# Performance work log

Hardware: AMD Instinct MI355X
Metric: run time of the kernel (lower is better)

Reference implementation:

```python
import jax, jax.numpy as jnp
import numpy as np
import math

C = 128
LAM = 0.25
MARGIN = 0.3
TAU = math.log(C)
B = 8192


def lambertw(z, iters=10):
    """Principal-branch Lambert W via Halley iterations (valid for z >= -1/e)."""
    e = jnp.exp(1.0)
    # series init near the branch point z = -1/e, log init for z >= 0
    p = jnp.sqrt(jnp.maximum(2.0 * (e * z + 1.0), 0.0))
    w_near = -1.0 + p - p * p / 3.0 + (11.0 / 72.0) * p ** 3
    w = jnp.where(z < 0.0, w_near, jnp.log1p(jnp.maximum(z, 0.0)))
    for _ in range(iters):
        ew = jnp.exp(w)
        f = w * ew - z
        wp1 = w + 1.0
        w = w - f / (ew * wp1 - (w + 2.0) * f / (2.0 * wp1))
    return w


def triplet_loss(x, targets):
    # pairwise euclidean distances [B, B]
    sq = jnp.sum(x * x, axis=1)
    dist = sq[:, None] + sq[None, :] - 2.0 * (x @ x.T)
    dist = jnp.sqrt(jnp.maximum(dist, 1e-12))
    pos = targets[:, None] == targets[None, :]
    # hardest positive / hardest negative per anchor
    dist_ap = jnp.max(jnp.where(pos, dist, -jnp.inf), axis=1)
    dist_an = jnp.min(jnp.where(pos, jnp.inf, dist), axis=1)
    # MarginRankingLoss(margin)(dist_an, dist_ap, y=1), mean reduction
    return jnp.mean(jnp.maximum(dist_ap - dist_an + MARGIN, 0.0))


def cross_entropy(logits, targets):
    logp = jax.nn.log_softmax(logits, axis=-1)
    return -jnp.mean(jnp.take_along_axis(logp, targets[:, None], axis=1)[:, 0])


def setup_inputs() -> dict:
    key = jax.random.key(0)
    k1, k2 = jax.random.split(key)
    logits = jax.random.normal(k1, (B, C), dtype=jnp.float32)
    targets = jax.random.randint(k2, (B,), 0, C, dtype=jnp.int64)
    return {"logits": logits, "targets": targets}


def reference(logits, targets):
    # l_i is detached in the original (and sigma goes through numpy -> no grad)
    l_i = jax.lax.stop_gradient(triplet_loss(logits, targets))
    y = 0.5 * jnp.maximum(-2.0 / jnp.exp(1.0), (l_i - TAU) / LAM)
    sigma = jax.lax.stop_gradient(jnp.exp(-lambertw(y)))
    ce = cross_entropy(logits, targets)
    loss = (ce - TAU) * sigma + LAM * jnp.log(sigma) ** 2
    return jnp.sum(loss) / B
```

## Files before the change

kernel.cpp:

```cpp
#include <hip/hip_runtime.h>
#include <math.h>

#define NB 8192
#define NC 128
#define NJS 8
#define JPT 8

typedef float v4f __attribute__((ext_vector_type(4)));
typedef int   v8i __attribute__((ext_vector_type(8)));

__global__ __launch_bounds__(256) void k_prep(const float* __restrict__ x,
                                              const int* __restrict__ tgt,
                                              unsigned* __restrict__ xq,
                                              float* __restrict__ sq,
                                              float* __restrict__ ce,
                                              float* __restrict__ sums,
                                              unsigned* __restrict__ cnt) {
    int row = blockIdx.x * 8 + (threadIdx.x >> 5);
    int l = threadIdx.x & 31;
    float4 v = ((const float4*)(x + row * NC))[l];
    unsigned p = __builtin_amdgcn_cvt_pk_fp8_f32(v.x, v.y, 0, false);
    p = __builtin_amdgcn_cvt_pk_fp8_f32(v.z, v.w, p, true);
    xq[row * 32 + l] = p;

    float ss = fmaf(v.x, v.x, fmaf(v.y, v.y, fmaf(v.z, v.z, v.w * v.w)));
    float mx = fmaxf(fmaxf(v.x, v.y), fmaxf(v.z, v.w));
#pragma unroll
    for (int off = 16; off; off >>= 1) {
        ss += __shfl_xor(ss, off);
        mx = fmaxf(mx, __shfl_xor(mx, off));
    }
    float es = expf(v.x - mx) + expf(v.y - mx) + expf(v.z - mx) + expf(v.w - mx);
#pragma unroll
    for (int off = 16; off; off >>= 1) es += __shfl_xor(es, off);
    if (l == 0) {
        sq[row] = ss;
        ce[row] = mx + logf(es) - x[row * NC + tgt[row]];
    }
    if (blockIdx.x == 0 && threadIdx.x < 4) {
        if (threadIdx.x < 2) sums[threadIdx.x] = 0.0f;
        if (threadIdx.x == 2) *cnt = 0u;
    }
}

__global__ __launch_bounds__(256, 4) void k_trip(const unsigned char* __restrict__ xq,
                                                 const int* __restrict__ tgt,
                                                 const float* __restrict__ sq,
                                                 float* __restrict__ pmax,
                                                 float* __restrict__ pmin) {
    __shared__ unsigned char Bs[2][128 * 128];
    __shared__ float sqs[1024];
    __shared__ int   tjs[1024];

    const int tid = threadIdx.x;
    const int lane = tid & 63;
    const int w = tid >> 6;
    const int rh = w >> 1;
    const int ch = w & 1;
    const int i0 = blockIdx.x * 64;
    const int jbase = blockIdx.y * 1024;
    const int m = lane & 15;
    const int quad = lane >> 4;

    __builtin_amdgcn_global_load_lds(
        (const __attribute__((address_space(1))) unsigned*)((const unsigned*)(sq + jbase) + (w * 64 + lane) * 4),
        (__attribute__((address_space(3))) unsigned*)(sqs + w * 256),
        16, 0, 0);
    __builtin_amdgcn_global_load_lds(
        (const __attribute__((address_space(1))) unsigned*)((const unsigned*)(tgt + jbase) + (w * 64 + lane) * 4),
        (__attribute__((address_space(3))) unsigned*)(tjs + w * 256),
        16, 0, 0);

#pragma unroll
    for (int c = 0; c < 4; ++c) {
        int L = w * 256 + c * 64 + lane;
        int col = L >> 3, cc = L & 7;
        const unsigned char* src = xq + (size_t)(jbase + col) * 128 + ((cc ^ (col & 7)) << 4);
        __builtin_amdgcn_global_load_lds(
            (const __attribute__((address_space(1))) unsigned*)src,
            (__attribute__((address_space(3))) unsigned*)(&Bs[0][0] + (w * 256 + c * 64) * 16),
            16, 0, 0);
    }

    v8i a[2];
#pragma unroll
    for (int tm = 0; tm < 2; ++tm) {
        int row = i0 + rh * 32 + tm * 16 + m;
        a[tm] = *(const v8i*)(xq + (size_t)row * 128 + quad * 32);
    }

    int ti[2][4];
#pragma unroll
    for (int tm = 0; tm < 2; ++tm)
#pragma unroll
        for (int r = 0; r < 4; ++r)
            ti[tm][r] = tgt[i0 + rh * 32 + tm * 16 + quad * 4 + r];

    float mp[2][4], mn[2][4];
#pragma unroll
    for (int tm = 0; tm < 2; ++tm)
#pragma unroll
        for (int r = 0; r < 4; ++r) { mp[tm][r] = -3.0e38f; mn[tm][r] = 3.0e38f; }

#pragma unroll 2
    for (int jt = 0; jt < JPT; ++jt) {
        __syncthreads();

        if (jt + 1 < JPT) {
            int jn = jbase + (jt + 1) * 128;
            unsigned char* Bnxt = &Bs[(jt + 1) & 1][0];
#pragma unroll
            for (int c = 0; c < 4; ++c) {
                int L = w * 256 + c * 64 + lane;
                int col = L >> 3, cc = L & 7;
                const unsigned char* src = xq + (size_t)(jn + col) * 128 + ((cc ^ (col & 7)) << 4);
                __builtin_amdgcn_global_load_lds(
                    (const __attribute__((address_space(1))) unsigned*)src,
                    (__attribute__((address_space(3))) unsigned*)(Bnxt + (w * 256 + c * 64) * 16),
                    16, 0, 0);
            }
        }

        const unsigned char* Bcur = &Bs[jt & 1][0];

        float sqj[4]; int tj[4];
#pragma unroll
        for (int tn = 0; tn < 4; ++tn) {
            int cloc = jt * 128 + ch * 64 + tn * 16 + m;
            sqj[tn] = sqs[cloc];
            tj[tn] = tjs[cloc];
        }

        v8i b[4];
#pragma unroll
        for (int tn = 0; tn < 4; ++tn) {
            int col = ch * 64 + tn * 16 + m;
            int base = col * 128;
            int c0 = (((quad * 2) ^ (col & 7)) << 4);
            int c1 = (((quad * 2 + 1) ^ (col & 7)) << 4);
            *(int4*)&b[tn] = *(const int4*)(Bcur + base + c0);
            *((int4*)&b[tn] + 1) = *(const int4*)(Bcur + base + c1);
        }

        v4f acc[2][4];
        v4f z = {0.0f, 0.0f, 0.0f, 0.0f};
#pragma unroll
        for (int tm = 0; tm < 2; ++tm)
#pragma unroll
            for (int tn = 0; tn < 4; ++tn)
                acc[tm][tn] = __builtin_amdgcn_mfma_scale_f32_16x16x128_f8f6f4(
                    a[tm], b[tn], z, 0, 0, 0, 0x7f7f7f7f, 0, 0x7f7f7f7f);

#pragma unroll
        for (int tn = 0; tn < 4; ++tn) {
#pragma unroll
            for (int tm = 0; tm < 2; ++tm)
#pragma unroll
                for (int r = 0; r < 4; ++r) {
                    float v = fmaf(-2.0f, acc[tm][tn][r], sqj[tn]);
                    bool pos = (tj[tn] == ti[tm][r]);
                    mp[tm][r] = fmaxf(mp[tm][r], pos ? v : -3.0e38f);
                    mn[tm][r] = fminf(mn[tm][r], pos ? 3.0e38f : v);
                }
        }
    }

#pragma unroll
    for (int off = 1; off < 16; off <<= 1) {
#pragma unroll
        for (int tm = 0; tm < 2; ++tm)
#pragma unroll
            for (int r = 0; r < 4; ++r) {
                mp[tm][r] = fmaxf(mp[tm][r], __shfl_xor(mp[tm][r], off));
                mn[tm][r] = fminf(mn[tm][r], __shfl_xor(mn[tm][r], off));
            }
    }
    if (m == 0) {
        int slice = blockIdx.y * 2 + ch;
        float* pm = pmax + (size_t)slice * NB + i0 + rh * 32;
        float* pn = pmin + (size_t)slice * NB + i0 + rh * 32;
#pragma unroll
        for (int tm = 0; tm < 2; ++tm)
#pragma unroll
            for (int r = 0; r < 4; ++r) {
                int rr = tm * 16 + quad * 4 + r;
                pm[rr] = mp[tm][r];
                pn[rr] = mn[tm][r];
            }
    }
}

__global__ __launch_bounds__(256) void k_tail(const float* __restrict__ sq,
                                              const float* __restrict__ ce,
                                              const float* __restrict__ pmax,
                                              const float* __restrict__ pmin,
                                              float* __restrict__ sums,
                                              unsigned* __restrict__ cnt,
                                              float* __restrict__ out) {
    __shared__ float sh[4], sc[4];
    __shared__ unsigned lastFlag;
    const int tid = threadIdx.x;
    int i = blockIdx.x * 256 + tid;

    float vmax = -3.0e38f, vmin = 3.0e38f;
#pragma unroll
    for (int s = 0; s < 16; ++s) {
        vmax = fmaxf(vmax, pmax[s * NB + i]);
        vmin = fminf(vmin, pmin[s * NB + i]);
    }
    float sqi = sq[i];
    float ap = sqrtf(fmaxf(fmaxf(sqi + vmax, 0.0f), 1e-12f));
    float an = sqrtf(fmaxf(fmaxf(sqi + vmin, 0.0f), 1e-12f));
    float hs = fmaxf(ap - an + 0.3f, 0.0f);
    float cs = ce[i];
#pragma unroll
    for (int off = 32; off; off >>= 1) {
        hs += __shfl_xor(hs, off);
        cs += __shfl_xor(cs, off);
    }
    int wv = tid >> 6;
    if ((tid & 63) == 0) { sh[wv] = hs; sc[wv] = cs; }
    __syncthreads();
    if (tid == 0) {
        float H = sh[0] + sh[1] + sh[2] + sh[3];
        float Cs = sc[0] + sc[1] + sc[2] + sc[3];
        atomicAdd(sums + 0, H);
        atomicAdd(sums + 1, Cs);
        __threadfence();
        unsigned prev = atomicAdd(cnt, 1u);
        lastFlag = (prev == (unsigned)(gridDim.x - 1));
    }
    __syncthreads();
    if (!lastFlag || tid != 0) return;

    double H = (double)atomicAdd(sums + 0, 0.0f);
    double Cs = (double)atomicAdd(sums + 1, 0.0f);
    const double E = 2.71828182845904523536;
    const double TAU = log(128.0);
    const double LAMd = 0.25;
    double l = H / (double)NB;
    double cev = Cs / (double)NB;
    double y = 0.5 * fmax(-2.0 / E, (l - TAU) / LAMd);
    double p = sqrt(fmax(2.0 * (E * y + 1.0), 0.0));
    double wn = -1.0 + p - p * p / 3.0 + (11.0 / 72.0) * p * p * p;
    double wlw = (y < 0.0) ? wn : log1p(fmax(y, 0.0));
#pragma unroll
    for (int it = 0; it < 10; ++it) {
        double ew = exp(wlw);
        double f = wlw * ew - y;
        double wp1 = wlw + 1.0;
        wlw = wlw - f / (ew * wp1 - (wlw + 2.0) * f / (2.0 * wp1));
    }
    double sigma = exp(-wlw);
    double lg = log(sigma);
    double loss = (cev - TAU) * sigma + LAMd * lg * lg;
    out[0] = (float)(loss / (double)NB);
}

extern "C" void kernel_launch(void* const* d_in, const int* in_sizes, int n_in,
                              void* d_out, int out_size, void* d_ws, size_t ws_size,
                              hipStream_t stream) {
    const float* x = (const float*)d_in[0];
    const int* tgt = (const int*)d_in[1];
    float* out = (float*)d_out;

    unsigned char* xq = (unsigned char*)d_ws;
    float* sq = (float*)(xq + (size_t)NB * 128);
    float* ce = sq + NB;
    float* sums = ce + NB;
    unsigned* cnt = (unsigned*)(sums + 2);
    float* pmax = (float*)(cnt + 62);
    float* pmin = pmax + (size_t)16 * NB;

    k_prep<<<NB / 8, 256, 0, stream>>>(x, tgt, (unsigned*)xq, sq, ce, sums, cnt);
    dim3 grid(NB / 64, NJS);
    k_trip<<<grid, 256, 0, stream>>>(xq, tgt, sq, pmax, pmin);
    k_tail<<<NB / 256, 256, 0, stream>>>(sq, ce, pmax, pmin, sums, cnt, out);
}
```

Before: 83.90 us.

## Exploit distance-matrix symmetry to compute only the upper-triangle tiles

The triplet kernel now skips blocks below the diagonal and, for each computed tile, also reduces column-wise to produce the hardest positive and negative for the transposed anchors. These column partials go to a separate buffer that the tail kernel merges with the row partials. This roughly halves the MFMA and LDS work. In exchange it adds column reductions, cross-lane shuffles, a much larger partial buffer (256 slices) with more global writes and tail reads, and uneven per-block load.

Result: slower. 151.9 us (+81.0%).

```diff
diff --git a/kernel.cpp b/kernel.cpp
--- a/kernel.cpp
+++ b/kernel.cpp
@@ -3,8 +3,8 @@
 
 #define NB 8192
 #define NC 128
-#define NJS 8
-#define JPT 8
+#define NSL 16
+#define JPT 4
 
 typedef float v4f __attribute__((ext_vector_type(4)));
 typedef int   v8i __attribute__((ext_vector_type(8)));
@@ -46,30 +46,35 @@
 __global__ __launch_bounds__(256, 4) void k_trip(const unsigned char* __restrict__ xq,
                                                  const int* __restrict__ tgt,
                                                  const float* __restrict__ sq,
-                                                 float* __restrict__ pmax,
-                                                 float* __restrict__ pmin) {
+                                                 float* __restrict__ rmax,
+                                                 float* __restrict__ rmin,
+                                                 float* __restrict__ cmax,
+                                                 float* __restrict__ cmin) {
+    const int ib = blockIdx.x;
+    const int s = blockIdx.y;
+    if (ib < 8 * s) return;
+    const int jtmax = min(3, (ib - 8 * s) >> 1);
+
     __shared__ unsigned char Bs[2][128 * 128];
-    __shared__ float sqs[1024];
-    __shared__ int   tjs[1024];
+    __shared__ float sqs[512];
+    __shared__ int   tjs[512];
 
     const int tid = threadIdx.x;
     const int lane = tid & 63;
     const int w = tid >> 6;
     const int rh = w >> 1;
     const int ch = w & 1;
-    const int i0 = blockIdx.x * 64;
-    const int jbase = blockIdx.y * 1024;
+    const int i0 = ib * 64;
+    const int jbase = s * 512;
     const int m = lane & 15;
     const int quad = lane >> 4;
 
-    __builtin_amdgcn_global_load_lds(
-        (const __attribute__((address_space(1))) unsigned*)((const unsigned*)(sq + jbase) + (w * 64 + lane) * 4),
-        (__attribute__((address_space(3))) unsigned*)(sqs + w * 256),
-        16, 0, 0);
-    __builtin_amdgcn_global_load_lds(
-        (const __attribute__((address_space(1))) unsigned*)((const unsigned*)(tgt + jbase) + (w * 64 + lane) * 4),
-        (__attribute__((address_space(3))) unsigned*)(tjs + w * 256),
-        16, 0, 0);
+    if (tid < 128) {
+        float4 s4 = *(const float4*)(sq + jbase + tid * 4);
+        int4 t4 = *(const int4*)(tgt + jbase + tid * 4);
+        *(float4*)&sqs[tid * 4] = s4;
+        *(int4*)&tjs[tid * 4] = t4;
+    }
 
 #pragma unroll
     for (int c = 0; c < 4; ++c) {
@@ -90,11 +95,15 @@
     }
 
     int ti[2][4];
+    float sqr[2][4];
 #pragma unroll
     for (int tm = 0; tm < 2; ++tm)
 #pragma unroll
-        for (int r = 0; r < 4; ++r)
-            ti[tm][r] = tgt[i0 + rh * 32 + tm * 16 + quad * 4 + r];
+        for (int r = 0; r < 4; ++r) {
+            int row = i0 + rh * 32 + tm * 16 + quad * 4 + r;
+            ti[tm][r] = tgt[row];
+            sqr[tm][r] = sq[row];
+        }
 
     float mp[2][4], mn[2][4];
 #pragma unroll
@@ -102,11 +111,10 @@
 #pragma unroll
         for (int r = 0; r < 4; ++r) { mp[tm][r] = -3.0e38f; mn[tm][r] = 3.0e38f; }
 
-#pragma unroll 2
-    for (int jt = 0; jt < JPT; ++jt) {
+    for (int jt = 0; jt <= jtmax; ++jt) {
         __syncthreads();
 
-        if (jt + 1 < JPT) {
+        if (jt < jtmax) {
             int jn = jbase + (jt + 1) * 128;
             unsigned char* Bnxt = &Bs[(jt + 1) & 1][0];
 #pragma unroll
@@ -122,46 +130,64 @@
         }
 
         const unsigned char* Bcur = &Bs[jt & 1][0];
-
-        float sqj[4]; int tj[4];
+        const v4f z = {0.0f, 0.0f, 0.0f, 0.0f};
+
+        float cmx[4], cmn[4];
+#pragma unroll
+        for (int tn = 0; tn < 4; ++tn) { cmx[tn] = -3.0e38f; cmn[tn] = 3.0e38f; }
+
 #pragma unroll
         for (int tn = 0; tn < 4; ++tn) {
-            int cloc = jt * 128 + ch * 64 + tn * 16 + m;
-            sqj[tn] = sqs[cloc];
-            tj[tn] = tjs[cloc];
+            int cloc = ch * 64 + tn * 16 + m;
+            float sqj = sqs[jt * 128 + cloc];
+            int tj = tjs[jt * 128 + cloc];
+
+            v8i b;
+            int base = cloc * 128;
+            *(int4*)&b = *(const int4*)(Bcur + base + ((((quad * 2) ^ (cloc & 7))) << 4));
+            *((int4*)&b + 1) = *(const int4*)(Bcur + base + ((((quad * 2 + 1) ^ (cloc & 7))) << 4));
+
+            v4f acc0 = __builtin_amdgcn_mfma_scale_f32_16x16x128_f8f6f4(
+                a[0], b, z, 0, 0, 0, 0x7f7f7f7f, 0, 0x7f7f7f7f);
+            v4f acc1 = __builtin_amdgcn_mfma_scale_f32_16x16x128_f8f6f4(
+                a[1], b, z, 0, 0, 0, 0x7f7f7f7f, 0, 0x7f7f7f7f);
+
+#pragma unroll
+            for (int r = 0; r < 4; ++r) {
+                {
+                    float d2 = fmaf(-2.0f, acc0[r], sqj);
+                    bool pos = (tj == ti[0][r]);
+                    mp[0][r] = fmaxf(mp[0][r], pos ? d2 : -3.0e38f);
+                    mn[0][r] = fminf(mn[0][r], pos ? 3.0e38f : d2);
+                    float vc = fmaf(-2.0f, acc0[r], sqr[0][r]);
+                    cmx[tn] = fmaxf(cmx[tn], pos ? vc : -3.0e38f);
+                    cmn[tn] = fminf(cmn[tn], pos ? 3.0e38f : vc);
+                }
+                {
+                    float d2 = fmaf(-2.0f, acc1[r], sqj);
+                    bool pos = (tj == ti[1][r]);
+                    mp[1][r] = fmaxf(mp[1][r], pos ? d2 : -3.0e38f);
+                    mn[1][r] = fminf(mn[1][r], pos ? 3.0e38f : d2);
+                    float vc = fmaf(-2.0f, acc1[r], sqr[1][r]);
+                    cmx[tn] = fmaxf(cmx[tn], pos ? vc : -3.0e38f);
+                    cmn[tn] = fminf(cmn[tn], pos ? 3.0e38f : vc);
+                }
+            }
         }
 
-        v8i b[4];
 #pragma unroll
         for (int tn = 0; tn < 4; ++tn) {
-            int col = ch * 64 + tn * 16 + m;
-            int base = col * 128;
-            int c0 = (((quad * 2) ^ (col & 7)) << 4);
-            int c1 = (((quad * 2 + 1) ^ (col & 7)) << 4);
-            *(int4*)&b[tn] = *(const int4*)(Bcur + base + c0);
-            *((int4*)&b[tn] + 1) = *(const int4*)(Bcur + base + c1);
-        }
-
-        v4f acc[2][4];
-        v4f z = {0.0f, 0.0f, 0.0f, 0.0f};
-#pragma unroll
-        for (int tm = 0; tm < 2; ++tm)
-#pragma unroll
-            for (int tn = 0; tn < 4; ++tn)
-                acc[tm][tn] = __builtin_amdgcn_mfma_scale_f32_16x16x128_f8f6f4(
-                    a[tm], b[tn], z, 0, 0, 0, 0x7f7f7f7f, 0, 0x7f7f7f7f);
-
-#pragma unroll
-        for (int tn = 0; tn < 4; ++tn) {
-#pragma unroll
-            for (int tm = 0; tm < 2; ++tm)
-#pragma unroll
-                for (int r = 0; r < 4; ++r) {
-                    float v = fmaf(-2.0f, acc[tm][tn][r], sqj[tn]);
-                    bool pos = (tj[tn] == ti[tm][r]);
-                    mp[tm][r] = fmaxf(mp[tm][r], pos ? v : -3.0e38f);
-                    mn[tm][r] = fminf(mn[tm][r], pos ? 3.0e38f : v);
-                }
+            float x1 = cmx[tn], n1 = cmn[tn];
+            x1 = fmaxf(x1, __shfl_xor(x1, 16));
+            x1 = fmaxf(x1, __shfl_xor(x1, 32));
+            n1 = fminf(n1, __shfl_xor(n1, 16));
+            n1 = fminf(n1, __shfl_xor(n1, 32));
+            if (quad == 0) {
+                int jcol = jbase + jt * 128 + ch * 64 + tn * 16 + m;
+                int slice_c = (((ib - 8 * s - 2 * jt)) << 1) + rh;
+                cmax[(size_t)slice_c * NB + jcol] = x1;
+                cmin[(size_t)slice_c * NB + jcol] = n1;
+            }
         }
     }
 
@@ -176,9 +202,9 @@
             }
     }
     if (m == 0) {
-        int slice = blockIdx.y * 2 + ch;
-        float* pm = pmax + (size_t)slice * NB + i0 + rh * 32;
-        float* pn = pmin + (size_t)slice * NB + i0 + rh * 32;
+        int slice = s * 2 + ch;
+        float* pm = rmax + (size_t)slice * NB + i0 + rh * 32;
+        float* pn = rmin + (size_t)slice * NB + i0 + rh * 32;
 #pragma unroll
         for (int tm = 0; tm < 2; ++tm)
 #pragma unroll
@@ -192,8 +218,10 @@
 
 __global__ __launch_bounds__(256) void k_tail(const float* __restrict__ sq,
                                               const float* __restrict__ ce,
-                                              const float* __restrict__ pmax,
-                                              const float* __restrict__ pmin,
+                                              const float* __restrict__ rmax,
+                                              const float* __restrict__ rmin,
+                                              const float* __restrict__ cmax,
+                                              const float* __restrict__ cmin,
                                               float* __restrict__ sums,
                                               unsigned* __restrict__ cnt,
                                               float* __restrict__ out) {
@@ -203,10 +231,15 @@
     int i = blockIdx.x * 256 + tid;
 
     float vmax = -3.0e38f, vmin = 3.0e38f;
-#pragma unroll
-    for (int s = 0; s < 16; ++s) {
-        vmax = fmaxf(vmax, pmax[s * NB + i]);
-        vmin = fminf(vmin, pmin[s * NB + i]);
+    int nrow = 2 * (i >> 9) + 2;
+    for (int sl = 0; sl < nrow; ++sl) {
+        vmax = fmaxf(vmax, rmax[(size_t)sl * NB + i]);
+        vmin = fminf(vmin, rmin[(size_t)sl * NB + i]);
+    }
+    int ncol = (128 - 2 * (i >> 7)) << 1;
+    for (int sl = 0; sl < ncol; ++sl) {
+        vmax = fmaxf(vmax, cmax[(size_t)sl * NB + i]);
+        vmin = fminf(vmin, cmin[(size_t)sl * NB + i]);
     }
     float sqi = sq[i];
     float ap = sqrtf(fmaxf(fmaxf(sqi + vmax, 0.0f), 1e-12f));
@@ -269,11 +302,13 @@
     float* ce = sq + NB;
     float* sums = ce + NB;
     unsigned* cnt = (unsigned*)(sums + 2);
-    float* pmax = (float*)(cnt + 62);
-    float* pmin = pmax + (size_t)16 * NB;
+    float* rmax = (float*)(cnt + 62);
+    float* rmin = rmax + (size_t)32 * NB;
+    float* cmax = rmin + (size_t)32 * NB;
+    float* cmin = cmax + (size_t)256 * NB;
 
     k_prep<<<NB / 8, 256, 0, stream>>>(x, tgt, (unsigned*)xq, sq, ce, sums, cnt);
-    dim3 grid(NB / 64, NJS);
-    k_trip<<<grid, 256, 0, stream>>>(xq, tgt, sq, pmax, pmin);
-    k_tail<<<NB / 256, 256, 0, stream>>>(sq, ce, pmax, pmin, sums, cnt, out);
+    dim3 grid(NB / 64, NSL);
+    k_trip<<<grid, 256, 0, stream>>>(xq, tgt, sq, rmax, rmin, cmax, cmin);
+    k_tail<<<NB / 256, 256, 0, stream>>>(sq, ce, rmax, rmin, cmax, cmin, sums, cnt, out);
 }
```

## Load B tiles directly from global into registers, dropping LDS staging

Applied to the files above, without the earlier changes.

The triplet-distance kernel no longer stages B columns, squared norms and targets through double-buffered shared memory with async global-to-LDS copies and barriers. Each lane now reads its 32-byte fp8 B fragment, sq and target straight from global memory (mostly L2-resident) inside a fully unrolled loop. This removes the barriers and LDS traffic and lowers LDS use, which may raise occupancy. In exchange it adds redundant global loads across waves and exposes load latency without explicit prefetching.

After: 100.5 us. 19.8% more time.

```diff
diff --git a/kernel.cpp b/kernel.cpp
--- a/kernel.cpp
+++ b/kernel.cpp
@@ -48,10 +48,6 @@
                                                  const float* __restrict__ sq,
                                                  float* __restrict__ pmax,
                                                  float* __restrict__ pmin) {
-    __shared__ unsigned char Bs[2][128 * 128];
-    __shared__ float sqs[1024];
-    __shared__ int   tjs[1024];
-
     const int tid = threadIdx.x;
     const int lane = tid & 63;
     const int w = tid >> 6;
@@ -62,26 +58,6 @@
     const int m = lane & 15;
     const int quad = lane >> 4;
 
-    __builtin_amdgcn_global_load_lds(
-        (const __attribute__((address_space(1))) unsigned*)((const unsigned*)(sq + jbase) + (w * 64 + lane) * 4),
-        (__attribute__((address_space(3))) unsigned*)(sqs + w * 256),
-        16, 0, 0);
-    __builtin_amdgcn_global_load_lds(
-        (const __attribute__((address_space(1))) unsigned*)((const unsigned*)(tgt + jbase) + (w * 64 + lane) * 4),
-        (__attribute__((address_space(3))) unsigned*)(tjs + w * 256),
-        16, 0, 0);
-
-#pragma unroll
-    for (int c = 0; c < 4; ++c) {
-        int L = w * 256 + c * 64 + lane;
-        int col = L >> 3, cc = L & 7;
-        const unsigned char* src = xq + (size_t)(jbase + col) * 128 + ((cc ^ (col & 7)) << 4);
-        __builtin_amdgcn_global_load_lds(
-            (const __attribute__((address_space(1))) unsigned*)src,
-            (__attribute__((address_space(3))) unsigned*)(&Bs[0][0] + (w * 256 + c * 64) * 16),
-            16, 0, 0);
-    }
-
     v8i a[2];
 #pragma unroll
     for (int tm = 0; tm < 2; ++tm) {
@@ -102,66 +78,39 @@
 #pragma unroll
         for (int r = 0; r < 4; ++r) { mp[tm][r] = -3.0e38f; mn[tm][r] = 3.0e38f; }
 
-#pragma unroll 2
+    const v4f z = {0.0f, 0.0f, 0.0f, 0.0f};
+
+#pragma unroll
     for (int jt = 0; jt < JPT; ++jt) {
-        __syncthreads();
-
-        if (jt + 1 < JPT) {
-            int jn = jbase + (jt + 1) * 128;
-            unsigned char* Bnxt = &Bs[(jt + 1) & 1][0];
-#pragma unroll
-            for (int c = 0; c < 4; ++c) {
-                int L = w * 256 + c * 64 + lane;
-                int col = L >> 3, cc = L & 7;
-                const unsigned char* src = xq + (size_t)(jn + col) * 128 + ((cc ^ (col & 7)) << 4);
-                __builtin_amdgcn_global_load_lds(
-                    (const __attribute__((address_space(1))) unsigned*)src,
-                    (__attribute__((address_space(3))) unsigned*)(Bnxt + (w * 256 + c * 64) * 16),
-                    16, 0, 0);
+        int j0 = jbase + jt * 128;
+#pragma unroll
+        for (int tn = 0; tn < 4; ++tn) {
+            int col = j0 + ch * 64 + tn * 16 + m;
+
+            v8i b = *(const v8i*)(xq + (size_t)col * 128 + quad * 32);
+            float sqj = sq[col];
+            int tj = tgt[col];
+
+            v4f acc0 = __builtin_amdgcn_mfma_scale_f32_16x16x128_f8f6f4(
+                a[0], b, z, 0, 0, 0, 0x7f7f7f7f, 0, 0x7f7f7f7f);
+            v4f acc1 = __builtin_amdgcn_mfma_scale_f32_16x16x128_f8f6f4(
+                a[1], b, z, 0, 0, 0, 0x7f7f7f7f, 0, 0x7f7f7f7f);
+
+#pragma unroll
+            for (int r = 0; r < 4; ++r) {
+                {
+                    float v = fmaf(-2.0f, acc0[r], sqj);
+                    bool pos = (tj == ti[0][r]);
+                    mp[0][r] = fmaxf(mp[0][r], pos ? v : -3.0e38f);
+                    mn[0][r] = fminf(mn[0][r], pos ? 3.0e38f : v);
+                }
+                {
+                    float v = fmaf(-2.0f, acc1[r], sqj);
+                    bool pos = (tj == ti[1][r]);
+                    mp[1][r] = fmaxf(mp[1][r], pos ? v : -3.0e38f);
+                    mn[1][r] = fminf(mn[1][r], pos ? 3.0e38f : v);
+                }
             }
-        }
-
-        const unsigned char* Bcur = &Bs[jt & 1][0];
-
-        float sqj[4]; int tj[4];
-#pragma unroll
-        for (int tn = 0; tn < 4; ++tn) {
-            int cloc = jt * 128 + ch * 64 + tn * 16 + m;
-            sqj[tn] = sqs[cloc];
-            tj[tn] = tjs[cloc];
-        }
-
-        v8i b[4];
-#pragma unroll
-        for (int tn = 0; tn < 4; ++tn) {
-            int col = ch * 64 + tn * 16 + m;
-            int base = col * 128;
-            int c0 = (((quad * 2) ^ (col & 7)) << 4);
-            int c1 = (((quad * 2 + 1) ^ (col & 7)) << 4);
-            *(int4*)&b[tn] = *(const int4*)(Bcur + base + c0);
-            *((int4*)&b[tn] + 1) = *(const int4*)(Bcur + base + c1);
-        }
-
-        v4f acc[2][4];
-        v4f z = {0.0f, 0.0f, 0.0f, 0.0f};
-#pragma unroll
-        for (int tm = 0; tm < 2; ++tm)
-#pragma unroll
-            for (int tn = 0; tn < 4; ++tn)
-                acc[tm][tn] = __builtin_amdgcn_mfma_scale_f32_16x16x128_f8f6f4(
-                    a[tm], b[tn], z, 0, 0, 0, 0x7f7f7f7f, 0, 0x7f7f7f7f);
-
-#pragma unroll
-        for (int tn = 0; tn < 4; ++tn) {
-#pragma unroll
-            for (int tm = 0; tm < 2; ++tm)
-#pragma unroll
-                for (int r = 0; r < 4; ++r) {
-                    float v = fmaf(-2.0f, acc[tm][tn][r], sqj[tn]);
-                    bool pos = (tj[tn] == ti[tm][r]);
-                    mp[tm][r] = fmaxf(mp[tm][r], pos ? v : -3.0e38f);
-                    mn[tm][r] = fminf(mn[tm][r], pos ? 3.0e38f : v);
-                }
         }
     }
 
```
